# Kernel tuning notes

Measured on AMD Instinct MI355X. Metric: run time of the kernel, lower is better.

## Reference

```python
import jax, jax.numpy as jnp
import numpy as np

B, N, D, H = 128, 512, 128, 8
DH = D // H
CLIP = 10.0          # tanh_clipping
NEG = -1.0e9         # finite -inf for masking (keeps grads clean)


def setup_inputs() -> dict:
    key = jax.random.key(0)
    ks = jax.random.split(key, 6)
    s = 0.08  # ~1/sqrt(D) init scale so pre-tanh logits are in a sane range
    return {
        "embeddings": jax.random.normal(ks[0], (B, N, D), jnp.float32),
        "W_node_proj": jax.random.normal(ks[1], (D, 3 * D), jnp.float32) * s,
        "W_fixed_ctx": jax.random.normal(ks[2], (D, D), jnp.float32) * s,
        "W_step_ctx": jax.random.normal(ks[3], (2 * D, D), jnp.float32) * s,
        "W_out": jax.random.normal(ks[4], (D, D), jnp.float32) * s,
        "W_placeholder": jax.random.uniform(ks[5], (2 * D,), jnp.float32, -1.0, 1.0),
    }


def reference(embeddings, W_node_proj, W_fixed_ctx, W_step_ctx, W_out, W_placeholder):
    # _precompute: fixed context + glimpse K/V + logit key (cached for all steps)
    graph_embed = embeddings.mean(axis=1)                    # [B,D]
    fixed_ctx = graph_embed @ W_fixed_ctx                    # [B,D]
    proj = embeddings @ W_node_proj                          # [B,N,3D]
    gK, gV, logit_K = jnp.split(proj, 3, axis=-1)
    gK = gK.reshape(B, N, H, DH)                             # glimpse key heads
    gV = gV.reshape(B, N, H, DH)                             # glimpse val heads
    inv_sqrt_dh = 1.0 / jnp.sqrt(jnp.float32(DH))
    inv_sqrt_d = 1.0 / jnp.sqrt(jnp.float32(D))
    batch_idx = jnp.arange(B)

    def step(carry, _):
        visited, first, prev, i = carry
        # step context: placeholder at i==0, else concat(first, current) embeddings
        cur_ctx = jnp.concatenate(
            [embeddings[batch_idx, first], embeddings[batch_idx, prev]], axis=-1)  # [B,2D]
        step_ctx = jnp.where(i == 0, W_placeholder[None, :], cur_ctx)
        q = fixed_ctx + step_ctx @ W_step_ctx                # [B,D]
        qh = q.reshape(B, H, DH)
        # masked multi-head glimpse attention
        compat = jnp.einsum('bhd,bnhd->bhn', qh, gK) * inv_sqrt_dh
        compat = jnp.where(visited[:, None, :], NEG, compat)
        attn = jax.nn.softmax(compat, axis=-1)
        heads = jnp.einsum('bhn,bnhd->bhd', attn, gV)
        glimpse = heads.reshape(B, D) @ W_out                # project_out
        # logit attention with tanh clipping
        logits = jnp.einsum('bd,bnd->bn', glimpse, logit_K) * inv_sqrt_d
        logits = CLIP * jnp.tanh(logits)
        logits = jnp.where(visited, NEG, logits)
        log_p = jax.nn.log_softmax(logits, axis=-1)
        sel = jnp.argmax(log_p, axis=-1).astype(jnp.int32)   # greedy decode
        visited = visited.at[batch_idx, sel].set(True)
        first = jnp.where(i == 0, sel, first)
        return (visited, first, sel, i + 1), (log_p, sel)

    init = (jnp.zeros((B, N), bool), jnp.zeros((B,), jnp.int32),
            jnp.zeros((B,), jnp.int32), jnp.int32(0))
    _, (log_ps, pis) = jax.lax.scan(step, init, None, length=N)
    log_p = jnp.transpose(log_ps, (1, 0, 2))                 # [B,N_steps,N]
    pi = jnp.transpose(pis, (1, 0))                          # [B,N_steps]
    # _calc_log_likelihood
    ll = jnp.take_along_axis(log_p, pi[:, :, None], axis=2).squeeze(-1).sum(axis=1)
    return log_p, pi, ll
```

## Files before the change

kernel.cpp:

```cpp
#include <hip/hip_runtime.h>
#include <hip/hip_bf16.h>
#include <math.h>

#define BATCH 128
#define NN 512
#define DD 128
#define D3 384
#define NEGV (-1.0e9f)
#define NEGINF (-1.0e30f)

__global__ __launch_bounds__(256) void k_fixed(const float* __restrict__ emb,
                                               const float* __restrict__ Wf,
                                               const float* __restrict__ Wstep,
                                               const float* __restrict__ Wph,
                                               float* __restrict__ fixedc,
                                               float* __restrict__ q0) {
  const int b = blockIdx.x;
  __shared__ float s_part[2][DD];
  __shared__ float s_ge[DD];
  const int tid = threadIdx.x;
  const int d = tid & 127, c = tid >> 7;
  const float* e = emb + (size_t)b * NN * DD;
  float acc = 0.f;
  for (int n = c * 256; n < c * 256 + 256; ++n) acc += e[(size_t)n * DD + d];
  s_part[c][d] = acc;
  __syncthreads();
  if (tid < DD) s_ge[tid] = (s_part[0][tid] + s_part[1][tid]) * (1.0f / 512.0f);
  __syncthreads();
  if (tid < DD) {
    float a = 0.f;
    for (int k = 0; k < DD; ++k) a += s_ge[k] * Wf[k * DD + tid];
    fixedc[b * DD + tid] = a;
    float pq = 0.f;
    for (int k = 0; k < 2 * DD; ++k) pq += Wph[k] * Wstep[k * DD + tid];
    q0[b * DD + tid] = a + pq;
  }
}

__global__ __launch_bounds__(384) void k_proj(const float* __restrict__ emb,
                                              const float* __restrict__ Wp,
                                              float* __restrict__ proj) {
  const size_t row0 = (size_t)blockIdx.x * 32;
  __shared__ float s_A[32][DD];
  const int tid = threadIdx.x;
  for (int t = tid; t < 32 * DD; t += 384)
    s_A[t >> 7][t & 127] = emb[row0 * DD + t];
  __syncthreads();
  float acc[32];
#pragma unroll
  for (int r = 0; r < 32; ++r) acc[r] = 0.f;
  const int c = tid;
  for (int k = 0; k < DD; ++k) {
    float w = Wp[k * D3 + c];
#pragma unroll
    for (int r = 0; r < 32; ++r) acc[r] += s_A[r][k] * w;
  }
  for (int r = 0; r < 32; ++r) proj[(row0 + r) * D3 + c] = acc[r];
}

__global__ __launch_bounds__(128) void k_lp(float* __restrict__ proj,
                                            const float* __restrict__ Wout) {
  const size_t row0 = (size_t)blockIdx.x * 32;
  __shared__ float s_L[32][DD];
  const int tid = threadIdx.x;
  for (int rr = 0; rr < 32; ++rr)
    s_L[rr][tid] = proj[(row0 + rr) * D3 + 2 * DD + tid];
  __syncthreads();
  float acc[32];
#pragma unroll
  for (int r = 0; r < 32; ++r) acc[r] = 0.f;
  for (int d = 0; d < DD; ++d) {
    const float w = Wout[tid * DD + d];
#pragma unroll
    for (int r = 0; r < 32; ++r) acc[r] += w * s_L[r][d];
  }
  for (int r = 0; r < 32; ++r)
    proj[(row0 + r) * D3 + 2 * DD + tid] = acc[r];
}

__global__ __launch_bounds__(256) void k_ectx(const float* __restrict__ emb,
                                              const float* __restrict__ Wstep,
                                              const float* __restrict__ fixedc,
                                              float* __restrict__ E12) {
  const size_t row0 = (size_t)blockIdx.x * 32;
  __shared__ float s_A[32][DD];
  const int tid = threadIdx.x;
  for (int t = tid; t < 32 * DD; t += 256)
    s_A[t >> 7][t & 127] = emb[row0 * DD + t];
  __syncthreads();
  float acc[32];
#pragma unroll
  for (int r = 0; r < 32; ++r) acc[r] = 0.f;
  const int c = tid;
  const int b = (int)(row0 >> 9);
  const float* wp = (c < DD) ? (Wstep + c) : (Wstep + DD * DD + (c - DD));
  for (int k = 0; k < DD; ++k) {
    float w = wp[(size_t)k * DD];
#pragma unroll
    for (int r = 0; r < 32; ++r) acc[r] += s_A[r][k] * w;
  }
  const float fc = (c < DD) ? fixedc[b * DD + c] : 0.f;
  for (int r = 0; r < 32; ++r) E12[(row0 + r) * 256 + c] = acc[r] + fc;
}

#define DOT16(q, F)                                                           \
  (q[0] * F[0].x + q[1] * F[0].y + q[2] * F[0].z + q[3] * F[0].w +            \
   q[4] * F[1].x + q[5] * F[1].y + q[6] * F[1].z + q[7] * F[1].w +            \
   q[8] * F[2].x + q[9] * F[2].y + q[10] * F[2].z + q[11] * F[2].w +          \
   q[12] * F[3].x + q[13] * F[3].y + q[14] * F[3].z + q[15] * F[3].w)

#define L_LOAD(njx, Lr)                                                       \
  {                                                                           \
    const float4* lp_ =                                                       \
        (const float4*)(projb + (size_t)(njx)*D3 + 2 * DD + h * 16);          \
    Lr[0] = lp_[0]; Lr[1] = lp_[1]; Lr[2] = lp_[2]; Lr[3] = lp_[3];           \
  }

#define L_CONSUME(Lr, njx)                                                    \
  {                                                                           \
    float a_ = DOT16(gf, Lr);                                                 \
    a_ += __shfl_xor(a_, 1);                                                  \
    a_ += __shfl_xor(a_, 2);                                                  \
    a_ += __shfl_xor(a_, 4);                                                  \
    if (h == 0) {                                                             \
      const float lg_ = 10.0f * tanhf(a_ * inv_sqrt_d);                       \
      s_logits[njx] = lg_;                                                    \
      asum += expf(lg_);                                                      \
      if (lg_ > av || (lg_ == av && (njx) < ai)) { av = lg_; ai = (njx); }    \
    }                                                                         \
  }

__global__ __launch_bounds__(1024, 1) void k_decode(
    const float* __restrict__ emb, const float* __restrict__ proj,
    const float* __restrict__ fixedc, const float* __restrict__ q0,
    const float* __restrict__ E12, const float* __restrict__ Wstep,
    const float* __restrict__ Wph, const int useE, float* __restrict__ out) {
  const int b = blockIdx.x;
  const int tid = threadIdx.x;
  const int lane = tid & 63;
  const int wave = tid >> 6;
  const int h = tid & 7, r = tid >> 3;

  __shared__ float4 s_Lpf[2][4][16][64];
  __shared__ int s_idx[NN];
  __shared__ int s_pos[NN];
  __shared__ unsigned char s_visited[NN];
  __shared__ float s_hacc[16][8][17];
  __shared__ float s_heads[DD];
  __shared__ float s_logits[NN];
  __shared__ float s_rm[16];
  __shared__ int s_ri[16];
  __shared__ float s_es[16];
  __shared__ float s_q[DD];
  __shared__ float s_ctx[2 * DD];
  __shared__ int s_first, s_prev, s_M, s_swap;
  __shared__ float s_ll, s_lzv;

  const float inv_sqrt_d = 0.08838834764831845f;
  const size_t eb = (size_t)b * NN * DD;
  const size_t e2 = (size_t)b * NN * 256;
  const float* projb = proj + (size_t)b * NN * D3;
  float* outp = out + (size_t)b * NN * NN;
  const size_t PI_OFF = (size_t)BATCH * NN * NN;
  const size_t LL_OFF = PI_OFF + (size_t)BATCH * NN;

  if (tid < NN) {
    s_idx[tid] = tid;
    s_pos[tid] = tid;
    s_visited[tid] = 0;
  }
  if (tid == 0) { s_first = 0; s_prev = 0; s_ll = 0.f; s_M = NN; }
#pragma unroll
  for (int s = 0; s < 2; ++s) {
    const float4* lp =
        (const float4*)(projb + (size_t)(r + s * 128) * D3 + 2 * DD + h * 16);
    s_Lpf[s][0][wave][lane] = lp[0];
    s_Lpf[s][1][wave][lane] = lp[1];
    s_Lpf[s][2][wave][lane] = lp[2];
    s_Lpf[s][3][wave][lane] = lp[3];
  }
  __syncthreads();

  for (int i = 0; i < NN; ++i) {
    const int M = s_M;
    const int first = s_first, prev = s_prev;

    float qf[16];
    if (useE) {
      if (i == 0) {
#pragma unroll
        for (int d = 0; d < 4; ++d) {
          const float4 v = *(const float4*)(q0 + b * DD + h * 16 + d * 4);
          qf[d * 4 + 0] = v.x; qf[d * 4 + 1] = v.y;
          qf[d * 4 + 2] = v.z; qf[d * 4 + 3] = v.w;
        }
      } else {
        const float* e1p = E12 + e2 + (size_t)first * 256 + h * 16;
        const float* e2p = E12 + e2 + (size_t)prev * 256 + DD + h * 16;
#pragma unroll
        for (int d = 0; d < 4; ++d) {
          const float4 a = *(const float4*)(e1p + d * 4);
          const float4 c = *(const float4*)(e2p + d * 4);
          qf[d * 4 + 0] = a.x + c.x;
          qf[d * 4 + 1] = a.y + c.y;
          qf[d * 4 + 2] = a.z + c.z;
          qf[d * 4 + 3] = a.w + c.w;
        }
      }
    } else {
      if (tid < 2 * DD) {
        float v;
        if (i == 0)
          v = Wph[tid];
        else
          v = (tid < DD) ? emb[eb + (size_t)first * DD + tid]
                         : emb[eb + (size_t)prev * DD + (tid - DD)];
        s_ctx[tid] = v;
      }
      __syncthreads();
      if (tid < DD) {
        float a = fixedc[b * DD + tid];
        for (int k = 0; k < 2 * DD; ++k) a += s_ctx[k] * Wstep[k * DD + tid];
        s_q[tid] = a;
      }
      __syncthreads();
#pragma unroll
      for (int d = 0; d < 16; ++d) qf[d] = s_q[h * 16 + d];
    }

    bool act[4];
    int nj[4];
#pragma unroll
    for (int k = 0; k < 4; ++k) {
      const int j = r + k * 128;
      act[k] = (j < M);
      nj[k] = s_idx[j];
    }
    float s_l = 0.f;
    float acc[16];
#pragma unroll
    for (int d = 0; d < 16; ++d) acc[d] = 0.f;
#pragma unroll
    for (int k = 0; k < 4; ++k) {
      if (act[k]) {
        const float* rp = projb + (size_t)nj[k] * D3 + h * 16;
        const float4* kp = (const float4*)rp;
        float4 k0 = kp[0], k1 = kp[1], k2 = kp[2], k3 = kp[3];
        float a = qf[0] * k0.x + qf[1] * k0.y + qf[2] * k0.z + qf[3] * k0.w +
                  qf[4] * k1.x + qf[5] * k1.y + qf[6] * k1.z + qf[7] * k1.w +
                  qf[8] * k2.x + qf[9] * k2.y + qf[10] * k2.z + qf[11] * k2.w +
                  qf[12] * k3.x + qf[13] * k3.y + qf[14] * k3.z +
                  qf[15] * k3.w;
        const float p = expf(a * 0.25f);
        s_l += p;
        const float4* vp = (const float4*)(rp + DD);
        float4 v0 = vp[0], v1 = vp[1], v2 = vp[2], v3 = vp[3];
        acc[0] += p * v0.x;  acc[1] += p * v0.y;
        acc[2] += p * v0.z;  acc[3] += p * v0.w;
        acc[4] += p * v1.x;  acc[5] += p * v1.y;
        acc[6] += p * v1.z;  acc[7] += p * v1.w;
        acc[8] += p * v2.x;  acc[9] += p * v2.y;
        acc[10] += p * v2.z; acc[11] += p * v2.w;
        acc[12] += p * v3.x; acc[13] += p * v3.y;
        acc[14] += p * v3.z; acc[15] += p * v3.w;
      }
    }
    {
      const bool k1 = (lane & 8) == 0;
#pragma unroll
      for (int d = 0; d < 8; ++d) {
        const float send = k1 ? acc[d + 8] : acc[d];
        const float got = __shfl_xor(send, 8);
        acc[d] = (k1 ? acc[d] : acc[d + 8]) + got;
      }
      const bool k2 = (lane & 16) == 0;
#pragma unroll
      for (int d = 0; d < 4; ++d) {
        const float send = k2 ? acc[d + 4] : acc[d];
        const float got = __shfl_xor(send, 16);
        acc[d] = (k2 ? acc[d] : acc[d + 4]) + got;
      }
      const bool k3 = (lane & 32) == 0;
#pragma unroll
      for (int d = 0; d < 2; ++d) {
        const float send = k3 ? acc[d + 2] : acc[d];
        const float got = __shfl_xor(send, 32);
        acc[d] = (k3 ? acc[d] : acc[d + 2]) + got;
      }
    }
    s_l += __shfl_xor(s_l, 8);
    s_l += __shfl_xor(s_l, 16);
    s_l += __shfl_xor(s_l, 32);
    {
      const int dim0 = ((lane & 8) ? 8 : 0) | ((lane & 16) ? 4 : 0) |
                       ((lane & 32) ? 2 : 0);
      s_hacc[wave][h][dim0] = acc[0];
      s_hacc[wave][h][dim0 + 1] = acc[1];
      if (lane < 8) s_hacc[wave][lane][16] = s_l;
    }
    float4 Lf2[4], Lf3[4];
    {
      const int j2 = r + 256, j3 = r + 384;
      const int nj2p = s_idx[(j2 < M) ? j2 : (M - 1)];
      const int nj3p = s_idx[(j3 < M) ? j3 : (M - 1)];
      L_LOAD(nj2p, Lf2);
      L_LOAD(nj3p, Lf3);
    }
    __syncthreads();

    if (tid < DD) {
      const int hh = tid >> 4, dh = tid & 15;
      float num = 0.f, den = 0.f;
#pragma unroll
      for (int w = 0; w < 16; ++w) {
        num += s_hacc[w][hh][dh];
        den += s_hacc[w][hh][16];
      }
      s_heads[tid] = num / den;
    } else if (tid >= 512) {
      const int t2 = tid - 512;
      if (s_visited[t2]) s_logits[t2] = NEGV;
    }
    __syncthreads();

    float gf[16];
#pragma unroll
    for (int d = 0; d < 16; ++d) gf[d] = s_heads[h * 16 + d];
    float av = NEGINF;
    int ai = 0x7FFFFFFF;
    float asum = 0.f;
    if (act[0]) {
      float4 LA[4];
      LA[0] = s_Lpf[0][0][wave][lane];
      LA[1] = s_Lpf[0][1][wave][lane];
      LA[2] = s_Lpf[0][2][wave][lane];
      LA[3] = s_Lpf[0][3][wave][lane];
      L_CONSUME(LA, nj[0]);
    }
    if (act[1]) {
      float4 LA[4];
      LA[0] = s_Lpf[1][0][wave][lane];
      LA[1] = s_Lpf[1][1][wave][lane];
      LA[2] = s_Lpf[1][2][wave][lane];
      LA[3] = s_Lpf[1][3][wave][lane];
      L_CONSUME(LA, nj[1]);
    }
    if (act[2]) { L_CONSUME(Lf2, nj[2]); }
    if (act[3]) { L_CONSUME(Lf3, nj[3]); }
#pragma unroll
    for (int off = 1; off <= 32; off <<= 1) {
      const float ov = __shfl_xor(av, off);
      const int oi = __shfl_xor(ai, off);
      asum += __shfl_xor(asum, off);
      if (ov > av || (ov == av && oi < ai)) { av = ov; ai = oi; }
    }
    if (lane == 0) { s_rm[wave] = av; s_ri[wave] = ai; s_es[wave] = asum; }
    __syncthreads();

    if (wave == 0) {
      float cv = (lane < 16) ? s_rm[lane] : NEGINF;
      int ci = (lane < 16) ? s_ri[lane] : 0x7FFFFFFF;
      float cs = (lane < 16) ? s_es[lane] : 0.f;
#pragma unroll
      for (int off = 1; off <= 8; off <<= 1) {
        const float ov = __shfl_xor(cv, off);
        const int oi = __shfl_xor(ci, off);
        cs += __shfl_xor(cs, off);
        if (ov > cv || (ov == cv && oi < ci)) { cv = ov; ci = oi; }
      }
      if (lane == 0) {
        const float lzv = logf(cs);
        const int sel = ci;
        s_lzv = lzv;
        s_ll += s_logits[sel] - lzv;
        s_visited[sel] = 1;
        if (i == 0) s_first = sel;
        s_prev = sel;
        out[PI_OFF + (size_t)b * NN + i] = (float)sel;
        const int p = s_pos[sel];
        const int last = s_idx[M - 1];
        s_idx[p] = last;
        s_pos[last] = p;
        s_idx[M - 1] = sel;
        s_pos[sel] = M - 1;
        s_M = M - 1;
        s_swap = p;
      }
    }
    __syncthreads();

    {
      const int sp = s_swap;
      if (sp < 256 && r == (sp & 127)) {
        const int sl = sp >> 7;
        const int nr = s_idx[sp];
        const float4* lp =
            (const float4*)(projb + (size_t)nr * D3 + 2 * DD + h * 16);
        s_Lpf[sl][0][wave][lane] = lp[0];
        s_Lpf[sl][1][wave][lane] = lp[1];
        s_Lpf[sl][2][wave][lane] = lp[2];
        s_Lpf[sl][3][wave][lane] = lp[3];
      }
    }
    const float lz = s_lzv;
    if (tid < NN) outp[(size_t)i * NN + tid] = s_logits[tid] - lz;
  }
  if (tid == 0) out[LL_OFF + b] = s_ll;
}

extern "C" void kernel_launch(void* const* d_in, const int* in_sizes, int n_in,
                              void* d_out, int out_size, void* d_ws,
                              size_t ws_size, hipStream_t stream) {
  const float* emb = (const float*)d_in[0];
  const float* Wnp = (const float*)d_in[1];
  const float* Wf = (const float*)d_in[2];
  const float* Wstep = (const float*)d_in[3];
  const float* Wout = (const float*)d_in[4];
  const float* Wph = (const float*)d_in[5];
  float* out = (float*)d_out;

  const size_t projN = (size_t)BATCH * NN * D3;
  const size_t eN = (size_t)BATCH * NN * 256;
  const size_t need_full = (projN + eN + 2 * (size_t)BATCH * DD) * 4;

  float* proj = (float*)d_ws;
  float* E12 = proj + projN;
  const int useE = (ws_size >= need_full) ? 1 : 0;
  float* fixedc = useE ? (E12 + eN) : (proj + projN);
  float* q0 = fixedc + (size_t)BATCH * DD;

  k_fixed<<<BATCH, 256, 0, stream>>>(emb, Wf, Wstep, Wph, fixedc, q0);
  k_proj<<<(BATCH * NN) / 32, 384, 0, stream>>>(emb, Wnp, proj);
  k_lp<<<(BATCH * NN) / 32, 128, 0, stream>>>(proj, Wout);
  if (useE) k_ectx<<<(BATCH * NN) / 32, 256, 0, stream>>>(emb, Wstep, fixedc, E12);
  k_decode<<<BATCH, 1024, 0, stream>>>(emb, proj, fixedc, q0,
                                       useE ? E12 : nullptr, Wstep, Wph, useE,
                                       out);
}
```

Measured before the change: 5.807 ms.

## Keep logits in registers and write output directly; use relaxed LDS-only barriers

```diff
diff --git a/kernel.cpp b/kernel.cpp
--- a/kernel.cpp
+++ b/kernel.cpp
@@ -116,19 +116,24 @@
     Lr[0] = lp_[0]; Lr[1] = lp_[1]; Lr[2] = lp_[2]; Lr[3] = lp_[3];           \
   }
 
-#define L_CONSUME(Lr, njx)                                                    \
+#define L_CONSUME(Lr, njx, LGR)                                               \
   {                                                                           \
     float a_ = DOT16(gf, Lr);                                                 \
     a_ += __shfl_xor(a_, 1);                                                  \
     a_ += __shfl_xor(a_, 2);                                                  \
     a_ += __shfl_xor(a_, 4);                                                  \
     if (h == 0) {                                                             \
-      const float lg_ = 10.0f * tanhf(a_ * inv_sqrt_d);                       \
-      s_logits[njx] = lg_;                                                    \
-      asum += expf(lg_);                                                      \
-      if (lg_ > av || (lg_ == av && (njx) < ai)) { av = lg_; ai = (njx); }    \
+      LGR = 10.0f * tanhf(a_ * inv_sqrt_d);                                   \
+      asum += expf(LGR);                                                      \
+      if (LGR > av || (LGR == av && (njx) < ai)) { av = LGR; ai = (njx); }    \
     }                                                                         \
   }
+
+__device__ __forceinline__ void barrier_rlx() {
+  asm volatile("s_waitcnt lgkmcnt(0)" ::: "memory");
+  __builtin_amdgcn_s_barrier();
+  asm volatile("" ::: "memory");
+}
 
 __global__ __launch_bounds__(1024, 1) void k_decode(
     const float* __restrict__ emb, const float* __restrict__ proj,
@@ -147,7 +152,6 @@
   __shared__ unsigned char s_visited[NN];
   __shared__ float s_hacc[16][8][17];
   __shared__ float s_heads[DD];
-  __shared__ float s_logits[NN];
   __shared__ float s_rm[16];
   __shared__ int s_ri[16];
   __shared__ float s_es[16];
@@ -306,7 +310,7 @@
       L_LOAD(nj2p, Lf2);
       L_LOAD(nj3p, Lf3);
     }
-    __syncthreads();
+    barrier_rlx();
 
     if (tid < DD) {
       const int hh = tid >> 4, dh = tid & 15;
@@ -317,11 +321,8 @@
         den += s_hacc[w][hh][16];
       }
       s_heads[tid] = num / den;
-    } else if (tid >= 512) {
-      const int t2 = tid - 512;
-      if (s_visited[t2]) s_logits[t2] = NEGV;
-    }
-    __syncthreads();
+    }
+    barrier_rlx();
 
     float gf[16];
 #pragma unroll
@@ -329,13 +330,14 @@
     float av = NEGINF;
     int ai = 0x7FFFFFFF;
     float asum = 0.f;
+    float lgr0 = 0.f, lgr1 = 0.f, lgr2 = 0.f, lgr3 = 0.f;
     if (act[0]) {
       float4 LA[4];
       LA[0] = s_Lpf[0][0][wave][lane];
       LA[1] = s_Lpf[0][1][wave][lane];
       LA[2] = s_Lpf[0][2][wave][lane];
       LA[3] = s_Lpf[0][3][wave][lane];
-      L_CONSUME(LA, nj[0]);
+      L_CONSUME(LA, nj[0], lgr0);
     }
     if (act[1]) {
       float4 LA[4];
@@ -343,10 +345,11 @@
       LA[1] = s_Lpf[1][1][wave][lane];
       LA[2] = s_Lpf[1][2][wave][lane];
       LA[3] = s_Lpf[1][3][wave][lane];
-      L_CONSUME(LA, nj[1]);
-    }
-    if (act[2]) { L_CONSUME(Lf2, nj[2]); }
-    if (act[3]) { L_CONSUME(Lf3, nj[3]); }
+      L_CONSUME(LA, nj[1], lgr1);
+    }
+    if (act[2]) { L_CONSUME(Lf2, nj[2], lgr2); }
+    if (act[3]) { L_CONSUME(Lf3, nj[3], lgr3); }
+    const int visn = (tid < NN) ? (int)s_visited[tid] : 0;
 #pragma unroll
     for (int off = 1; off <= 32; off <<= 1) {
       const float ov = __shfl_xor(av, off);
@@ -355,7 +358,7 @@
       if (ov > av || (ov == av && oi < ai)) { av = ov; ai = oi; }
     }
     if (lane == 0) { s_rm[wave] = av; s_ri[wave] = ai; s_es[wave] = asum; }
-    __syncthreads();
+    barrier_rlx();
 
     if (wave == 0) {
       float cv = (lane < 16) ? s_rm[lane] : NEGINF;
@@ -372,7 +375,7 @@
         const float lzv = logf(cs);
         const int sel = ci;
         s_lzv = lzv;
-        s_ll += s_logits[sel] - lzv;
+        s_ll += cv - lzv;
         s_visited[sel] = 1;
         if (i == 0) s_first = sel;
         s_prev = sel;
@@ -387,7 +390,7 @@
         s_swap = p;
       }
     }
-    __syncthreads();
+    barrier_rlx();
 
     {
       const int sp = s_swap;
@@ -403,7 +406,13 @@
       }
     }
     const float lz = s_lzv;
-    if (tid < NN) outp[(size_t)i * NN + tid] = s_logits[tid] - lz;
+    if (h == 0) {
+      if (act[0]) outp[(size_t)i * NN + nj[0]] = lgr0 - lz;
+      if (act[1]) outp[(size_t)i * NN + nj[1]] = lgr1 - lz;
+      if (act[2]) outp[(size_t)i * NN + nj[2]] = lgr2 - lz;
+      if (act[3]) outp[(size_t)i * NN + nj[3]] = lgr3 - lz;
+    }
+    if (tid < NN && visn) outp[(size_t)i * NN + tid] = NEGV - lz;
   }
   if (tid == 0) out[LL_OFF + b] = s_ll;
 }
```

Measured after the change: 5.842 ms. About the same (+0.6%).

## Split each batch decode across two workgroups with global-memory flag handshakes

Applied to the files above, without the earlier changes.

```diff
diff --git a/kernel.cpp b/kernel.cpp
--- a/kernel.cpp
+++ b/kernel.cpp
@@ -8,6 +8,9 @@
 #define D3 384
 #define NEGV (-1.0e9f)
 #define NEGINF (-1.0e30f)
+
+#define COMM_STRIDE 304
+#define COMM_F (256 + BATCH * COMM_STRIDE)
 
 __global__ __launch_bounds__(256) void k_fixed(const float* __restrict__ emb,
                                                const float* __restrict__ Wf,
@@ -109,45 +112,54 @@
    q[8] * F[2].x + q[9] * F[2].y + q[10] * F[2].z + q[11] * F[2].w +          \
    q[12] * F[3].x + q[13] * F[3].y + q[14] * F[3].z + q[15] * F[3].w)
 
-#define L_LOAD(njx, Lr)                                                       \
-  {                                                                           \
-    const float4* lp_ =                                                       \
-        (const float4*)(projb + (size_t)(njx)*D3 + 2 * DD + h * 16);          \
-    Lr[0] = lp_[0]; Lr[1] = lp_[1]; Lr[2] = lp_[2]; Lr[3] = lp_[3];           \
-  }
-
-#define L_CONSUME(Lr, njx)                                                    \
-  {                                                                           \
-    float a_ = DOT16(gf, Lr);                                                 \
-    a_ += __shfl_xor(a_, 1);                                                  \
-    a_ += __shfl_xor(a_, 2);                                                  \
-    a_ += __shfl_xor(a_, 4);                                                  \
-    if (h == 0) {                                                             \
-      const float lg_ = 10.0f * tanhf(a_ * inv_sqrt_d);                       \
-      s_logits[njx] = lg_;                                                    \
-      asum += expf(lg_);                                                      \
-      if (lg_ > av || (lg_ == av && (njx) < ai)) { av = lg_; ai = (njx); }    \
-    }                                                                         \
-  }
+__device__ __forceinline__ int ld_acq_i(int* p) {
+  return __hip_atomic_load(p, __ATOMIC_ACQUIRE, __HIP_MEMORY_SCOPE_AGENT);
+}
+__device__ __forceinline__ void st_rel_i(int* p, int v) {
+  __hip_atomic_store(p, v, __ATOMIC_RELEASE, __HIP_MEMORY_SCOPE_AGENT);
+}
+__device__ __forceinline__ float ld_f(float* p) {
+  return __hip_atomic_load(p, __ATOMIC_RELAXED, __HIP_MEMORY_SCOPE_AGENT);
+}
+__device__ __forceinline__ void st_f(float* p, float v) {
+  __hip_atomic_store(p, v, __ATOMIC_RELAXED, __HIP_MEMORY_SCOPE_AGENT);
+}
+__device__ __forceinline__ int ld_i(int* p) {
+  return __hip_atomic_load(p, __ATOMIC_RELAXED, __HIP_MEMORY_SCOPE_AGENT);
+}
+__device__ __forceinline__ void st_i(int* p, int v) {
+  __hip_atomic_store(p, v, __ATOMIC_RELAXED, __HIP_MEMORY_SCOPE_AGENT);
+}
 
 __global__ __launch_bounds__(1024, 1) void k_decode(
     const float* __restrict__ emb, const float* __restrict__ proj,
     const float* __restrict__ fixedc, const float* __restrict__ q0,
     const float* __restrict__ E12, const float* __restrict__ Wstep,
-    const float* __restrict__ Wph, const int useE, float* __restrict__ out) {
-  const int b = blockIdx.x;
+    const float* __restrict__ Wph, const int useE, float* __restrict__ out,
+    float* __restrict__ comm, int* __restrict__ flags) {
+  const int x = blockIdx.x;
+  const int half = (x >> 3) & 1;
+  const int b = (x & 7) | ((x >> 4) << 3);
   const int tid = threadIdx.x;
   const int lane = tid & 63;
   const int wave = tid >> 6;
-  const int h = tid & 7, r = tid >> 3;
-
-  __shared__ float4 s_Lpf[2][4][16][64];
+  const int h = tid & 7, rr = tid >> 3;
+
+  float* bc = comm + (size_t)b * COMM_STRIDE;
+  float* mynd = bc + half * 144;
+  float* pnd = bc + (1 - half) * 144;
+  float* mytri = bc + 288 + half * 8;
+  float* ptri = bc + 288 + (1 - half) * 8;
+  int* myflag = flags + b * 2 + half;
+  int* pflag = flags + b * 2 + (1 - half);
+
+  __shared__ float4 s_Lpf[2][4][1024];
   __shared__ int s_idx[NN];
   __shared__ int s_pos[NN];
   __shared__ unsigned char s_visited[NN];
   __shared__ float s_hacc[16][8][17];
+  __shared__ float s_numden[136];
   __shared__ float s_heads[DD];
-  __shared__ float s_logits[NN];
   __shared__ float s_rm[16];
   __shared__ int s_ri[16];
   __shared__ float s_es[16];
@@ -171,13 +183,14 @@
   }
   if (tid == 0) { s_first = 0; s_prev = 0; s_ll = 0.f; s_M = NN; }
 #pragma unroll
-  for (int s = 0; s < 2; ++s) {
+  for (int k = 0; k < 2; ++k) {
+    const int p = 2 * (rr + 128 * k) + half;
     const float4* lp =
-        (const float4*)(projb + (size_t)(r + s * 128) * D3 + 2 * DD + h * 16);
-    s_Lpf[s][0][wave][lane] = lp[0];
-    s_Lpf[s][1][wave][lane] = lp[1];
-    s_Lpf[s][2][wave][lane] = lp[2];
-    s_Lpf[s][3][wave][lane] = lp[3];
+        (const float4*)(projb + (size_t)p * D3 + 2 * DD + h * 16);
+    s_Lpf[k][0][tid] = lp[0];
+    s_Lpf[k][1][tid] = lp[1];
+    s_Lpf[k][2][tid] = lp[2];
+    s_Lpf[k][3][tid] = lp[3];
   }
   __syncthreads();
 
@@ -228,43 +241,42 @@
       for (int d = 0; d < 16; ++d) qf[d] = s_q[h * 16 + d];
     }
 
-    bool act[4];
-    int nj[4];
-#pragma unroll
-    for (int k = 0; k < 4; ++k) {
-      const int j = r + k * 128;
-      act[k] = (j < M);
-      nj[k] = s_idx[j];
-    }
+    const int j0 = 2 * rr + half;
+    const int j1 = 2 * (rr + 128) + half;
+    const bool act0 = (j0 < M), act1 = (j1 < M);
+    const int nj0 = s_idx[j0], nj1 = s_idx[j1];
+
     float s_l = 0.f;
     float acc[16];
 #pragma unroll
     for (int d = 0; d < 16; ++d) acc[d] = 0.f;
-#pragma unroll
-    for (int k = 0; k < 4; ++k) {
-      if (act[k]) {
-        const float* rp = projb + (size_t)nj[k] * D3 + h * 16;
-        const float4* kp = (const float4*)rp;
-        float4 k0 = kp[0], k1 = kp[1], k2 = kp[2], k3 = kp[3];
-        float a = qf[0] * k0.x + qf[1] * k0.y + qf[2] * k0.z + qf[3] * k0.w +
-                  qf[4] * k1.x + qf[5] * k1.y + qf[6] * k1.z + qf[7] * k1.w +
-                  qf[8] * k2.x + qf[9] * k2.y + qf[10] * k2.z + qf[11] * k2.w +
-                  qf[12] * k3.x + qf[13] * k3.y + qf[14] * k3.z +
-                  qf[15] * k3.w;
-        const float p = expf(a * 0.25f);
-        s_l += p;
-        const float4* vp = (const float4*)(rp + DD);
-        float4 v0 = vp[0], v1 = vp[1], v2 = vp[2], v3 = vp[3];
-        acc[0] += p * v0.x;  acc[1] += p * v0.y;
-        acc[2] += p * v0.z;  acc[3] += p * v0.w;
-        acc[4] += p * v1.x;  acc[5] += p * v1.y;
-        acc[6] += p * v1.z;  acc[7] += p * v1.w;
-        acc[8] += p * v2.x;  acc[9] += p * v2.y;
-        acc[10] += p * v2.z; acc[11] += p * v2.w;
-        acc[12] += p * v3.x; acc[13] += p * v3.y;
-        acc[14] += p * v3.z; acc[15] += p * v3.w;
-      }
-    }
+#define KV_SLOT(ACT, NJ)                                                      \
+    if (ACT) {                                                                \
+      const float* rp = projb + (size_t)(NJ)*D3 + h * 16;                     \
+      const float4* kp = (const float4*)rp;                                   \
+      float4 k0 = kp[0], k1 = kp[1], k2 = kp[2], k3 = kp[3];                  \
+      float a = qf[0] * k0.x + qf[1] * k0.y + qf[2] * k0.z + qf[3] * k0.w +   \
+                qf[4] * k1.x + qf[5] * k1.y + qf[6] * k1.z + qf[7] * k1.w +   \
+                qf[8] * k2.x + qf[9] * k2.y + qf[10] * k2.z + qf[11] * k2.w + \
+                qf[12] * k3.x + qf[13] * k3.y + qf[14] * k3.z +               \
+                qf[15] * k3.w;                                                \
+      const float p = expf(a * 0.25f);                                        \
+      s_l += p;                                                               \
+      const float4* vp = (const float4*)(rp + DD);                            \
+      float4 v0 = vp[0], v1 = vp[1], v2 = vp[2], v3 = vp[3];                  \
+      acc[0] += p * v0.x;  acc[1] += p * v0.y;                                \
+      acc[2] += p * v0.z;  acc[3] += p * v0.w;                                \
+      acc[4] += p * v1.x;  acc[5] += p * v1.y;                                \
+      acc[6] += p * v1.z;  acc[7] += p * v1.w;                                \
+      acc[8] += p * v2.x;  acc[9] += p * v2.y;                                \
+      acc[10] += p * v2.z; acc[11] += p * v2.w;                               \
+      acc[12] += p * v3.x; acc[13] += p * v3.y;                               \
+      acc[14] += p * v3.z; acc[15] += p * v3.w;                               \
+    }
+    KV_SLOT(act0, nj0);
+    KV_SLOT(act1, nj1);
+#undef KV_SLOT
+
     {
       const bool k1 = (lane & 8) == 0;
 #pragma unroll
@@ -298,55 +310,77 @@
       s_hacc[wave][h][dim0 + 1] = acc[1];
       if (lane < 8) s_hacc[wave][lane][16] = s_l;
     }
-    float4 Lf2[4], Lf3[4];
-    {
-      const int j2 = r + 256, j3 = r + 384;
-      const int nj2p = s_idx[(j2 < M) ? j2 : (M - 1)];
-      const int nj3p = s_idx[(j3 < M) ? j3 : (M - 1)];
-      L_LOAD(nj2p, Lf2);
-      L_LOAD(nj3p, Lf3);
-    }
-    __syncthreads();
-
-    if (tid < DD) {
+    __syncthreads();
+
+    if (tid < 128) {
       const int hh = tid >> 4, dh = tid & 15;
-      float num = 0.f, den = 0.f;
-#pragma unroll
-      for (int w = 0; w < 16; ++w) {
-        num += s_hacc[w][hh][dh];
-        den += s_hacc[w][hh][16];
-      }
-      s_heads[tid] = num / den;
-    } else if (tid >= 512) {
-      const int t2 = tid - 512;
-      if (s_visited[t2]) s_logits[t2] = NEGV;
+      float num = 0.f;
+#pragma unroll
+      for (int w = 0; w < 16; ++w) num += s_hacc[w][hh][dh];
+      s_numden[tid] = num;
+      st_f(mynd + tid, num);
+      __threadfence();
+    } else if (tid < 136) {
+      const int hh = tid - 128;
+      float den = 0.f;
+#pragma unroll
+      for (int w = 0; w < 16; ++w) den += s_hacc[w][hh][16];
+      s_numden[tid] = den;
+      st_f(mynd + tid, den);
+      __threadfence();
+    }
+    __syncthreads();
+    if (tid == 0) {
+      st_rel_i(myflag, 2 * i + 1);
+      while (ld_acq_i(pflag) < 2 * i + 1) __builtin_amdgcn_s_sleep(1);
+    }
+    __syncthreads();
+
+    if (tid < 128) {
+      const float pn = ld_f(pnd + tid);
+      const float pd = ld_f(pnd + 128 + (tid >> 4));
+      s_heads[tid] = (s_numden[tid] + pn) / (s_numden[128 + (tid >> 4)] + pd);
     }
     __syncthreads();
 
     float gf[16];
 #pragma unroll
     for (int d = 0; d < 16; ++d) gf[d] = s_heads[h * 16 + d];
+    float aa0 = 0.f, aa1 = 0.f;
+    if (act0) {
+      float4 LA[4];
+      LA[0] = s_Lpf[0][0][tid]; LA[1] = s_Lpf[0][1][tid];
+      LA[2] = s_Lpf[0][2][tid]; LA[3] = s_Lpf[0][3][tid];
+      aa0 = DOT16(gf, LA);
+    }
+    if (act1) {
+      float4 LA[4];
+      LA[0] = s_Lpf[1][0][tid]; LA[1] = s_Lpf[1][1][tid];
+      LA[2] = s_Lpf[1][2][tid]; LA[3] = s_Lpf[1][3][tid];
+      aa1 = DOT16(gf, LA);
+    }
+#pragma unroll
+    for (int off = 1; off <= 4; off <<= 1) {
+      aa0 += __shfl_xor(aa0, off);
+      aa1 += __shfl_xor(aa1, off);
+    }
+    const int visn = (tid < NN) ? (int)s_visited[tid] : 0;
     float av = NEGINF;
     int ai = 0x7FFFFFFF;
     float asum = 0.f;
-    if (act[0]) {
-      float4 LA[4];
-      LA[0] = s_Lpf[0][0][wave][lane];
-      LA[1] = s_Lpf[0][1][wave][lane];
-      LA[2] = s_Lpf[0][2][wave][lane];
-      LA[3] = s_Lpf[0][3][wave][lane];
-      L_CONSUME(LA, nj[0]);
-    }
-    if (act[1]) {
-      float4 LA[4];
-      LA[0] = s_Lpf[1][0][wave][lane];
-      LA[1] = s_Lpf[1][1][wave][lane];
-      LA[2] = s_Lpf[1][2][wave][lane];
-      LA[3] = s_Lpf[1][3][wave][lane];
-      L_CONSUME(LA, nj[1]);
-    }
-    if (act[2]) { L_CONSUME(Lf2, nj[2]); }
-    if (act[3]) { L_CONSUME(Lf3, nj[3]); }
+    float lgr0 = 0.f, lgr1 = 0.f;
+    if (h == 0) {
+      if (act0) {
+        lgr0 = 10.0f * tanhf(aa0 * inv_sqrt_d);
+        asum += expf(lgr0);
+        if (lgr0 > av || (lgr0 == av && nj0 < ai)) { av = lgr0; ai = nj0; }
+      }
+      if (act1) {
+        lgr1 = 10.0f * tanhf(aa1 * inv_sqrt_d);
+        asum += expf(lgr1);
+        if (lgr1 > av || (lgr1 == av && nj1 < ai)) { av = lgr1; ai = nj1; }
+      }
+    }
 #pragma unroll
     for (int off = 1; off <= 32; off <<= 1) {
       const float ov = __shfl_xor(av, off);
@@ -369,14 +403,26 @@
         if (ov > cv || (ov == cv && oi < ci)) { cv = ov; ci = oi; }
       }
       if (lane == 0) {
-        const float lzv = logf(cs);
-        const int sel = ci;
+        st_f(mytri + 0, cv);
+        st_f(mytri + 1, cs);
+        st_i((int*)(mytri + 2), ci);
+        st_rel_i(myflag, 2 * i + 2);
+        while (ld_acq_i(pflag) < 2 * i + 2) __builtin_amdgcn_s_sleep(1);
+        const float ov = ld_f(ptri + 0);
+        const float os = ld_f(ptri + 1);
+        const int oi = ld_i((int*)(ptri + 2));
+        float bv = cv;
+        int bi = ci;
+        float bs = cs + os;
+        if (ov > bv || (ov == bv && oi < bi)) { bv = ov; bi = oi; }
+        const float lzv = logf(bs);
+        const int sel = bi;
         s_lzv = lzv;
-        s_ll += s_logits[sel] - lzv;
+        s_ll += bv - lzv;
         s_visited[sel] = 1;
         if (i == 0) s_first = sel;
         s_prev = sel;
-        out[PI_OFF + (size_t)b * NN + i] = (float)sel;
+        if (half == 0) out[PI_OFF + (size_t)b * NN + i] = (float)sel;
         const int p = s_pos[sel];
         const int last = s_idx[M - 1];
         s_idx[p] = last;
@@ -391,21 +437,30 @@
 
     {
       const int sp = s_swap;
-      if (sp < 256 && r == (sp & 127)) {
-        const int sl = sp >> 7;
-        const int nr = s_idx[sp];
-        const float4* lp =
-            (const float4*)(projb + (size_t)nr * D3 + 2 * DD + h * 16);
-        s_Lpf[sl][0][wave][lane] = lp[0];
-        s_Lpf[sl][1][wave][lane] = lp[1];
-        s_Lpf[sl][2][wave][lane] = lp[2];
-        s_Lpf[sl][3][wave][lane] = lp[3];
+      if ((sp & 1) == half && sp < M - 1) {
+        const int q = (sp - half) >> 1;
+        if ((tid >> 3) == (q & 127)) {
+          const int k = q >> 7;
+          const int nr = s_idx[sp];
+          const float4* lp =
+              (const float4*)(projb + (size_t)nr * D3 + 2 * DD + h * 16);
+          s_Lpf[k][0][tid] = lp[0];
+          s_Lpf[k][1][tid] = lp[1];
+          s_Lpf[k][2][tid] = lp[2];
+          s_Lpf[k][3][tid] = lp[3];
+        }
       }
     }
     const float lz = s_lzv;
-    if (tid < NN) outp[(size_t)i * NN + tid] = s_logits[tid] - lz;
-  }
-  if (tid == 0) out[LL_OFF + b] = s_ll;
+    if (h == 0) {
+      if (act0) outp[(size_t)i * NN + nj0] = lgr0 - lz;
+      if (act1) outp[(size_t)i * NN + nj1] = lgr1 - lz;
+    }
+    if (tid < NN && visn && ((tid & 1) == half))
+      outp[(size_t)i * NN + tid] = NEGV - lz;
+    __syncthreads();
+  }
+  if (tid == 0 && half == 0) out[LL_OFF + b] = s_ll;
 }
 
 extern "C" void kernel_launch(void* const* d_in, const int* in_sizes, int n_in,
@@ -421,19 +476,23 @@
 
   const size_t projN = (size_t)BATCH * NN * D3;
   const size_t eN = (size_t)BATCH * NN * 256;
-  const size_t need_full = (projN + eN + 2 * (size_t)BATCH * DD) * 4;
-
-  float* proj = (float*)d_ws;
+  const size_t need_full = (COMM_F + projN + eN + 2 * (size_t)BATCH * DD) * 4;
+
+  int* flags = (int*)d_ws;
+  float* comm = (float*)d_ws + 256;
+  float* proj = (float*)d_ws + COMM_F;
   float* E12 = proj + projN;
   const int useE = (ws_size >= need_full) ? 1 : 0;
   float* fixedc = useE ? (E12 + eN) : (proj + projN);
   float* q0 = fixedc + (size_t)BATCH * DD;
 
+  hipMemsetAsync(flags, 0, 256 * sizeof(int), stream);
   k_fixed<<<BATCH, 256, 0, stream>>>(emb, Wf, Wstep, Wph, fixedc, q0);
   k_proj<<<(BATCH * NN) / 32, 384, 0, stream>>>(emb, Wnp, proj);
   k_lp<<<(BATCH * NN) / 32, 128, 0, stream>>>(proj, Wout);
-  if (useE) k_ectx<<<(BATCH * NN) / 32, 256, 0, stream>>>(emb, Wstep, fixedc, E12);
-  k_decode<<<BATCH, 1024, 0, stream>>>(emb, proj, fixedc, q0,
-                                       useE ? E12 : nullptr, Wstep, Wph, useE,
-                                       out);
-}
+  if (useE)
+    k_ectx<<<(BATCH * NN) / 32, 256, 0, stream>>>(emb, Wstep, fixedc, E12);
+  k_decode<<<2 * BATCH, 1024, 0, stream>>>(emb, proj, fixedc, q0,
+                                           useE ? E12 : nullptr, Wstep, Wph,
+                                           useE, out, comm, flags);
+}
```

Result: slower. 20.80 ms (+258.2%).
